# Performance work log

Hardware: AMD Instinct MI355X
Metric: run time of the kernel (lower is better)

The kernel has to match this reference:

```python
import jax, jax.numpy as jnp
import numpy as np

B, S, D = 16, 2048, 128
NEG = -1e9


def setup_inputs() -> dict:
    key = jax.random.key(0)
    kq, kk, kv = jax.random.split(key, 3)
    queries = jax.random.normal(kq, (B, S, D), dtype=jnp.float32)
    keys = jax.random.normal(kk, (B, S, D), dtype=jnp.float32)
    values = jax.random.normal(kv, (B, S, D), dtype=jnp.float32)
    # causal additive mask: 0 on/below diagonal, -1e9 above
    causal = jnp.triu(jnp.ones((S, S), dtype=jnp.float32), k=1) * NEG
    return {"queries": queries, "keys": keys, "values": values, "mask": causal}


def reference(queries, keys, values, mask):
    d = queries.shape[-1]
    scale = 1.0 / jnp.sqrt(jnp.asarray(d, dtype=queries.dtype))
    # scores: [b, q, k]
    scores = jnp.einsum("bqd,bkd->bqk", queries, keys) * scale
    scores = scores + mask  # broadcast [S,S] over batch
    weights = jax.nn.softmax(scores, axis=-1)
    # dropout p=0.0 in eval mode -> identity
    return jnp.einsum("bqk,bkd->bqd", weights, values)
```

## Files before the change

### kernel.cpp

```cpp
#include <hip/hip_runtime.h>
#include <hip/hip_bf16.h>

#define SS   2048
#define DD   128
#define QBLK 64
#define KBLK 64

typedef __attribute__((ext_vector_type(8))) short short8;
typedef __attribute__((ext_vector_type(4))) float f32x4;

__device__ __forceinline__ unsigned short f2bf(float x) {
  return __builtin_bit_cast(unsigned short, (__bf16)x);
}

__device__ __forceinline__ int sigma_col(int a) {
  return (a & 35) | ((a & 12) << 1) | ((a & 16) >> 2);
}

__global__ __launch_bounds__(256) void sdpa_causal_kernel(
    const float* __restrict__ Q, const float* __restrict__ K,
    const float* __restrict__ V, float* __restrict__ O)
{
  __shared__ __align__(16) char smem[KBLK * DD * 2 + DD * KBLK * 2];
  char* Klds  = smem;
  char* Vtlds = smem + KBLK * DD * 2;

  const int b   = blockIdx.x;
  const int qb  = (int)gridDim.y - 1 - (int)blockIdx.y;
  const int q0  = qb * QBLK;
  const int tid = threadIdx.x;
  const int lane = tid & 63;
  const int wid  = tid >> 6;
  const int l15  = lane & 15;
  const int hi   = lane >> 4;

  const float* Qb = Q + (size_t)b * SS * DD;
  const float* Kb = K + (size_t)b * SS * DD;
  const float* Vb = V + (size_t)b * SS * DD;
  float*       Ob = O + (size_t)b * SS * DD;

  const float scale = 0.08838834764831845f;

  short8 qf[4];
  {
    const float* qrow = Qb + (size_t)(q0 + wid * 16 + l15) * DD;
    #pragma unroll
    for (int c = 0; c < 4; ++c) {
      const float4* p = reinterpret_cast<const float4*>(qrow + 32 * c + 8 * hi);
      float4 x = p[0], y = p[1];
      short8 w;
      w[0] = f2bf(x.x * scale); w[1] = f2bf(x.y * scale);
      w[2] = f2bf(x.z * scale); w[3] = f2bf(x.w * scale);
      w[4] = f2bf(y.x * scale); w[5] = f2bf(y.y * scale);
      w[6] = f2bf(y.z * scale); w[7] = f2bf(y.w * scale);
      qf[c] = w;
    }
  }

  f32x4 o[8];
  #pragma unroll
  for (int nt = 0; nt < 8; ++nt) o[nt] = (f32x4){0.f, 0.f, 0.f, 0.f};
  float m = -INFINITY;
  float lsum = 0.f;

  const int ntile = qb + 1;
  for (int t = 0; t < ntile; ++t) {
    const int kv0 = t * KBLK;
    if (t) __syncthreads();

    #pragma unroll
    for (int u = 0; u < 4; ++u) {
      int row = u * 16 + (tid >> 4);
      int col = 8 * (tid & 15);
      const float4* sp = reinterpret_cast<const float4*>(Kb + (size_t)(kv0 + row) * DD + col);
      float4 x = sp[0], y = sp[1];
      short8 w;
      w[0] = f2bf(x.x); w[1] = f2bf(x.y); w[2] = f2bf(x.z); w[3] = f2bf(x.w);
      w[4] = f2bf(y.x); w[5] = f2bf(y.y); w[6] = f2bf(y.z); w[7] = f2bf(y.w);
      int byteoff = row * 256 + col * 2;
      byteoff ^= (row & 7) << 4;
      *reinterpret_cast<short8*>(Klds + byteoff) = w;
    }
    #pragma unroll
    for (int u = 0; u < 4; ++u) {
      int row = u * 16 + (tid >> 4);
      int col = 8 * (tid & 15);
      const float4* sp = reinterpret_cast<const float4*>(Vb + (size_t)(kv0 + row) * DD + col);
      float4 x = sp[0], y = sp[1];
      int sc = sigma_col(row);
      float vals[8] = {x.x, x.y, x.z, x.w, y.x, y.y, y.z, y.w};
      #pragma unroll
      for (int j = 0; j < 8; ++j) {
        int d = col + j;
        int byteoff = (d << 7) + (sc << 1);
        byteoff ^= (((d >> 3) ^ d) & 7) << 4;
        *reinterpret_cast<unsigned short*>(Vtlds + byteoff) = f2bf(vals[j]);
      }
    }
    __syncthreads();

    f32x4 sacc[4];
    #pragma unroll
    for (int g = 0; g < 4; ++g) {
      f32x4 acc = {0.f, 0.f, 0.f, 0.f};
      #pragma unroll
      for (int c = 0; c < 4; ++c) {
        int row = g * 16 + l15;
        int byteoff = row * 256 + (32 * c + 8 * hi) * 2;
        byteoff ^= (row & 7) << 4;
        short8 kf = *reinterpret_cast<const short8*>(Klds + byteoff);
        acc = __builtin_amdgcn_mfma_f32_16x16x32_bf16(kf, qf[c], acc, 0, 0, 0);
      }
      sacc[g] = acc;
    }

    if (t == ntile - 1) {
      const int q = q0 + wid * 16 + l15;
      #pragma unroll
      for (int g = 0; g < 4; ++g)
        #pragma unroll
        for (int i = 0; i < 4; ++i) {
          int key = kv0 + g * 16 + 4 * hi + i;
          if (key > q) sacc[g][i] = -1e30f;
        }
    }

    float tmax = -INFINITY;
    #pragma unroll
    for (int g = 0; g < 4; ++g)
      #pragma unroll
      for (int i = 0; i < 4; ++i) tmax = fmaxf(tmax, sacc[g][i]);
    tmax = fmaxf(tmax, __shfl_xor(tmax, 16));
    tmax = fmaxf(tmax, __shfl_xor(tmax, 32));
    float mnew = fmaxf(m, tmax);
    float corr = __expf(m - mnew);
    m = mnew;

    float p[4][4];
    float psum = 0.f;
    #pragma unroll
    for (int g = 0; g < 4; ++g)
      #pragma unroll
      for (int i = 0; i < 4; ++i) {
        float pv = __expf(sacc[g][i] - mnew);
        p[g][i] = pv;
        psum += pv;
      }
    psum += __shfl_xor(psum, 16);
    psum += __shfl_xor(psum, 32);
    lsum = lsum * corr + psum;

    float corrO[4];
    #pragma unroll
    for (int i = 0; i < 4; ++i) corrO[i] = __shfl(corr, 4 * hi + i);
    #pragma unroll
    for (int nt = 0; nt < 8; ++nt)
      #pragma unroll
      for (int i = 0; i < 4; ++i) o[nt][i] *= corrO[i];

    short8 pf[2];
    #pragma unroll
    for (int ks = 0; ks < 2; ++ks) {
      short8 w;
      #pragma unroll
      for (int i = 0; i < 4; ++i) {
        w[i]     = f2bf(p[2 * ks][i]);
        w[4 + i] = f2bf(p[2 * ks + 1][i]);
      }
      pf[ks] = w;
    }

    #pragma unroll
    for (int ks = 0; ks < 2; ++ks) {
      #pragma unroll
      for (int nt = 0; nt < 8; ++nt) {
        int d = nt * 16 + l15;
        int byteoff = (d << 7) + (ks * 32 + 8 * hi) * 2;
        byteoff ^= (((d >> 3) ^ d) & 7) << 4;
        short8 vf = *reinterpret_cast<const short8*>(Vtlds + byteoff);
        o[nt] = __builtin_amdgcn_mfma_f32_16x16x32_bf16(pf[ks], vf, o[nt], 0, 0, 0);
      }
    }
  }

  float rl = 1.0f / lsum;
  float rlO[4];
  #pragma unroll
  for (int i = 0; i < 4; ++i) rlO[i] = __shfl(rl, 4 * hi + i);
  const int qrow = q0 + wid * 16;
  #pragma unroll
  for (int nt = 0; nt < 8; ++nt)
    #pragma unroll
    for (int i = 0; i < 4; ++i)
      Ob[(size_t)(qrow + 4 * hi + i) * DD + nt * 16 + l15] = o[nt][i] * rlO[i];
}

extern "C" void kernel_launch(void* const* d_in, const int* in_sizes, int n_in,
                              void* d_out, int out_size, void* d_ws, size_t ws_size,
                              hipStream_t stream) {
  const float* Q = (const float*)d_in[0];
  const float* K = (const float*)d_in[1];
  const float* V = (const float*)d_in[2];
  float* O = (float*)d_out;

  dim3 grid(16, SS / QBLK);
  dim3 block(256);
  sdpa_causal_kernel<<<grid, block, 0, stream>>>(Q, K, V, O);
}
```

Measured before the change: 71.96 us.

## Prepack K/V to bf16 swizzled tiles and double-buffer async LDS loads

A prepass kernel converts K and V to bf16 once per call and writes them into workspace in the LDS-swizzled layout, with V already transposed. The attention kernel then copies tiles straight into LDS with global_load_lds, double-buffered so the next tile loads while the current one computes. It also reorders the q-block schedule and raises wave priority around the MFMA sections. This removes the conversion and transpose work that was repeated per query block, at the cost of an extra launch and workspace traffic, and it only runs when the workspace is large enough.

```diff
diff --git a/kernel.cpp b/kernel.cpp
--- a/kernel.cpp
+++ b/kernel.cpp
@@ -1,10 +1,14 @@
 #include <hip/hip_runtime.h>
 #include <hip/hip_bf16.h>
+#include <cstdint>
 
 #define SS   2048
 #define DD   128
 #define QBLK 64
 #define KBLK 64
+#define NTILES (SS / KBLK)
+#define TILE_BYTES 16384
+#define WS_NEED ((size_t)16 * NTILES * TILE_BYTES * 2)
 
 typedef __attribute__((ext_vector_type(8))) short short8;
 typedef __attribute__((ext_vector_type(4))) float f32x4;
@@ -15,6 +19,237 @@
 
 __device__ __forceinline__ int sigma_col(int a) {
   return (a & 35) | ((a & 12) << 1) | ((a & 16) >> 2);
+}
+
+__global__ __launch_bounds__(256) void prepack_kv(
+    const float* __restrict__ K, const float* __restrict__ V, char* __restrict__ ws)
+{
+  __shared__ float vf[64][129];
+  const int b = blockIdx.x, t = blockIdx.y;
+  const int tid = threadIdx.x;
+  const float* Kt = K + ((size_t)b * SS + t * KBLK) * DD;
+  const float* Vt = V + ((size_t)b * SS + t * KBLK) * DD;
+  char* Kd = ws + ((size_t)(b * NTILES + t)) * TILE_BYTES;
+  char* Vd = ws + (size_t)16 * NTILES * TILE_BYTES + ((size_t)(b * NTILES + t)) * TILE_BYTES;
+
+  #pragma unroll
+  for (int u = 0; u < 4; ++u) {
+    int row = u * 16 + (tid >> 4);
+    int col = 8 * (tid & 15);
+    const float4* sp = reinterpret_cast<const float4*>(Kt + (size_t)row * DD + col);
+    float4 x = sp[0], y = sp[1];
+    short8 w;
+    w[0] = f2bf(x.x); w[1] = f2bf(x.y); w[2] = f2bf(x.z); w[3] = f2bf(x.w);
+    w[4] = f2bf(y.x); w[5] = f2bf(y.y); w[6] = f2bf(y.z); w[7] = f2bf(y.w);
+    int off = (row * 256 + col * 2) ^ ((row & 7) << 4);
+    *reinterpret_cast<short8*>(Kd + off) = w;
+  }
+  #pragma unroll
+  for (int u = 0; u < 4; ++u) {
+    int row = u * 16 + (tid >> 4);
+    int col = 8 * (tid & 15);
+    const float4* sp = reinterpret_cast<const float4*>(Vt + (size_t)row * DD + col);
+    float4 x = sp[0], y = sp[1];
+    vf[row][col + 0] = x.x; vf[row][col + 1] = x.y; vf[row][col + 2] = x.z; vf[row][col + 3] = x.w;
+    vf[row][col + 4] = y.x; vf[row][col + 5] = y.y; vf[row][col + 6] = y.z; vf[row][col + 7] = y.w;
+  }
+  __syncthreads();
+  #pragma unroll
+  for (int q = 0; q < 4; ++q) {
+    int idx = q * 256 + tid;
+    int d = idx >> 3, y = idx & 7;
+    short8 w;
+    #pragma unroll
+    for (int j = 0; j < 8; ++j) {
+      int a = (j & 3) | ((y & 3) << 2) | ((j & 4) << 2) | ((y & 4) << 3);
+      w[j] = f2bf(vf[a][d]);
+    }
+    int off = ((d << 7) + (y << 4)) ^ ((((d >> 3) ^ d) & 7) << 4);
+    *reinterpret_cast<short8*>(Vd + off) = w;
+  }
+}
+
+__device__ __forceinline__ void stage_tile(const char* Ksrc, const char* Vsrc,
+                                           char* Kl, char* Vl, int wid, int lane)
+{
+  #pragma unroll
+  for (int i = 0; i < 4; ++i) {
+    int off = wid * 4096 + i * 1024;
+    __builtin_amdgcn_global_load_lds(
+        (const __attribute__((address_space(1))) unsigned int*)(Ksrc + off + lane * 16),
+        (__attribute__((address_space(3))) unsigned int*)(Kl + off), 16, 0, 0);
+  }
+  #pragma unroll
+  for (int i = 0; i < 4; ++i) {
+    int off = wid * 4096 + i * 1024;
+    __builtin_amdgcn_global_load_lds(
+        (const __attribute__((address_space(1))) unsigned int*)(Vsrc + off + lane * 16),
+        (__attribute__((address_space(3))) unsigned int*)(Vl + off), 16, 0, 0);
+  }
+}
+
+__global__ __launch_bounds__(256) void sdpa_causal_v2(
+    const float* __restrict__ Q, const char* __restrict__ ws, float* __restrict__ O)
+{
+  __shared__ __align__(16) char smem[2 * 32768];
+
+  const int b = blockIdx.x;
+  const int y = blockIdx.y;
+  const int qb = (y < 16) ? (31 - y) : (y - 16);
+  const int q0 = qb * QBLK;
+  const int tid = threadIdx.x;
+  const int lane = tid & 63;
+  const int wid  = tid >> 6;
+  const int l15  = lane & 15;
+  const int hi   = lane >> 4;
+
+  const float* Qb = Q + (size_t)b * SS * DD;
+  float*       Ob = O + (size_t)b * SS * DD;
+  const char*  Kws = ws + ((size_t)b * NTILES) * TILE_BYTES;
+  const char*  Vws = ws + (size_t)16 * NTILES * TILE_BYTES + ((size_t)b * NTILES) * TILE_BYTES;
+
+  const float scale = 0.08838834764831845f;
+
+  short8 qf[4];
+  {
+    const float* qrow = Qb + (size_t)(q0 + wid * 16 + l15) * DD;
+    #pragma unroll
+    for (int c = 0; c < 4; ++c) {
+      const float4* p = reinterpret_cast<const float4*>(qrow + 32 * c + 8 * hi);
+      float4 x = p[0], y2 = p[1];
+      short8 w;
+      w[0] = f2bf(x.x * scale); w[1] = f2bf(x.y * scale);
+      w[2] = f2bf(x.z * scale); w[3] = f2bf(x.w * scale);
+      w[4] = f2bf(y2.x * scale); w[5] = f2bf(y2.y * scale);
+      w[6] = f2bf(y2.z * scale); w[7] = f2bf(y2.w * scale);
+      qf[c] = w;
+    }
+  }
+
+  f32x4 o[8];
+  #pragma unroll
+  for (int nt = 0; nt < 8; ++nt) o[nt] = (f32x4){0.f, 0.f, 0.f, 0.f};
+  float m = -INFINITY;
+  float lsum = 0.f;
+
+  const int ntile = qb + 1;
+  int cur = 0;
+
+  stage_tile(Kws, Vws, smem, smem + 16384, wid, lane);
+  __syncthreads();
+
+  for (int t = 0; t < ntile; ++t) {
+    if (t + 1 < ntile) {
+      char* nb = smem + (cur ^ 1) * 32768;
+      stage_tile(Kws + (size_t)(t + 1) * TILE_BYTES, Vws + (size_t)(t + 1) * TILE_BYTES,
+                 nb, nb + 16384, wid, lane);
+    }
+
+    const char* Kl = smem + cur * 32768;
+    const char* Vl = Kl + 16384;
+    const int kv0 = t * KBLK;
+
+    f32x4 sacc[4];
+    __builtin_amdgcn_s_setprio(1);
+    #pragma unroll
+    for (int g = 0; g < 4; ++g) {
+      f32x4 acc = {0.f, 0.f, 0.f, 0.f};
+      #pragma unroll
+      for (int c = 0; c < 4; ++c) {
+        int row = g * 16 + l15;
+        int byteoff = (row * 256 + (32 * c + 8 * hi) * 2) ^ ((row & 7) << 4);
+        short8 kf = *reinterpret_cast<const short8*>(Kl + byteoff);
+        acc = __builtin_amdgcn_mfma_f32_16x16x32_bf16(kf, qf[c], acc, 0, 0, 0);
+      }
+      sacc[g] = acc;
+    }
+    __builtin_amdgcn_s_setprio(0);
+
+    if (t == ntile - 1) {
+      const int q = q0 + wid * 16 + l15;
+      #pragma unroll
+      for (int g = 0; g < 4; ++g)
+        #pragma unroll
+        for (int i = 0; i < 4; ++i) {
+          int key = kv0 + g * 16 + 4 * hi + i;
+          if (key > q) sacc[g][i] = -1e30f;
+        }
+    }
+
+    float tmax = -INFINITY;
+    #pragma unroll
+    for (int g = 0; g < 4; ++g)
+      #pragma unroll
+      for (int i = 0; i < 4; ++i) tmax = fmaxf(tmax, sacc[g][i]);
+    tmax = fmaxf(tmax, __shfl_xor(tmax, 16));
+    tmax = fmaxf(tmax, __shfl_xor(tmax, 32));
+    float mnew = fmaxf(m, tmax);
+    float corr = __expf(m - mnew);
+    m = mnew;
+
+    float p[4][4];
+    float psum = 0.f;
+    #pragma unroll
+    for (int g = 0; g < 4; ++g)
+      #pragma unroll
+      for (int i = 0; i < 4; ++i) {
+        float pv = __expf(sacc[g][i] - mnew);
+        p[g][i] = pv;
+        psum += pv;
+      }
+    psum += __shfl_xor(psum, 16);
+    psum += __shfl_xor(psum, 32);
+    lsum = lsum * corr + psum;
+
+    float corrO[4];
+    #pragma unroll
+    for (int i = 0; i < 4; ++i) corrO[i] = __shfl(corr, 4 * hi + i);
+    #pragma unroll
+    for (int nt = 0; nt < 8; ++nt)
+      #pragma unroll
+      for (int i = 0; i < 4; ++i) o[nt][i] *= corrO[i];
+
+    short8 pf[2];
+    #pragma unroll
+    for (int ks = 0; ks < 2; ++ks) {
+      short8 w;
+      #pragma unroll
+      for (int i = 0; i < 4; ++i) {
+        w[i]     = f2bf(p[2 * ks][i]);
+        w[4 + i] = f2bf(p[2 * ks + 1][i]);
+      }
+      pf[ks] = w;
+    }
+
+    __builtin_amdgcn_s_setprio(1);
+    #pragma unroll
+    for (int ks = 0; ks < 2; ++ks) {
+      #pragma unroll
+      for (int nt = 0; nt < 8; ++nt) {
+        int d = nt * 16 + l15;
+        int byteoff = ((d << 7) + (ks * 32 + 8 * hi) * 2) ^ ((((d >> 3) ^ d) & 7) << 4);
+        short8 vvf = *reinterpret_cast<const short8*>(Vl + byteoff);
+        o[nt] = __builtin_amdgcn_mfma_f32_16x16x32_bf16(pf[ks], vvf, o[nt], 0, 0, 0);
+      }
+    }
+    __builtin_amdgcn_s_setprio(0);
+
+    if (t + 1 < ntile) {
+      __syncthreads();
+      cur ^= 1;
+    }
+  }
+
+  float rl = 1.0f / lsum;
+  float rlO[4];
+  #pragma unroll
+  for (int i = 0; i < 4; ++i) rlO[i] = __shfl(rl, 4 * hi + i);
+  const int qrow = q0 + wid * 16;
+  #pragma unroll
+  for (int nt = 0; nt < 8; ++nt)
+    #pragma unroll
+    for (int i = 0; i < 4; ++i)
+      Ob[(size_t)(qrow + 4 * hi + i) * DD + nt * 16 + l15] = o[nt][i] * rlO[i];
 }
 
 __global__ __launch_bounds__(256) void sdpa_causal_kernel(
@@ -77,8 +312,7 @@
       short8 w;
       w[0] = f2bf(x.x); w[1] = f2bf(x.y); w[2] = f2bf(x.z); w[3] = f2bf(x.w);
       w[4] = f2bf(y.x); w[5] = f2bf(y.y); w[6] = f2bf(y.z); w[7] = f2bf(y.w);
-      int byteoff = row * 256 + col * 2;
-      byteoff ^= (row & 7) << 4;
+      int byteoff = (row * 256 + col * 2) ^ ((row & 7) << 4);
       *reinterpret_cast<short8*>(Klds + byteoff) = w;
     }
     #pragma unroll
@@ -92,8 +326,7 @@
       #pragma unroll
       for (int j = 0; j < 8; ++j) {
         int d = col + j;
-        int byteoff = (d << 7) + (sc << 1);
-        byteoff ^= (((d >> 3) ^ d) & 7) << 4;
+        int byteoff = ((d << 7) + (sc << 1)) ^ ((((d >> 3) ^ d) & 7) << 4);
         *reinterpret_cast<unsigned short*>(Vtlds + byteoff) = f2bf(vals[j]);
       }
     }
@@ -106,8 +339,7 @@
       #pragma unroll
       for (int c = 0; c < 4; ++c) {
         int row = g * 16 + l15;
-        int byteoff = row * 256 + (32 * c + 8 * hi) * 2;
-        byteoff ^= (row & 7) << 4;
+        int byteoff = (row * 256 + (32 * c + 8 * hi) * 2) ^ ((row & 7) << 4);
         short8 kf = *reinterpret_cast<const short8*>(Klds + byteoff);
         acc = __builtin_amdgcn_mfma_f32_16x16x32_bf16(kf, qf[c], acc, 0, 0, 0);
       }
@@ -175,10 +407,9 @@
       #pragma unroll
       for (int nt = 0; nt < 8; ++nt) {
         int d = nt * 16 + l15;
-        int byteoff = (d << 7) + (ks * 32 + 8 * hi) * 2;
-        byteoff ^= (((d >> 3) ^ d) & 7) << 4;
-        short8 vf = *reinterpret_cast<const short8*>(Vtlds + byteoff);
-        o[nt] = __builtin_amdgcn_mfma_f32_16x16x32_bf16(pf[ks], vf, o[nt], 0, 0, 0);
+        int byteoff = ((d << 7) + (ks * 32 + 8 * hi) * 2) ^ ((((d >> 3) ^ d) & 7) << 4);
+        short8 vvf = *reinterpret_cast<const short8*>(Vtlds + byteoff);
+        o[nt] = __builtin_amdgcn_mfma_f32_16x16x32_bf16(pf[ks], vvf, o[nt], 0, 0, 0);
       }
     }
   }
@@ -203,7 +434,11 @@
   const float* V = (const float*)d_in[2];
   float* O = (float*)d_out;
 
-  dim3 grid(16, SS / QBLK);
-  dim3 block(256);
-  sdpa_causal_kernel<<<grid, block, 0, stream>>>(Q, K, V, O);
-}
+  if (ws_size >= WS_NEED) {
+    char* ws = (char*)d_ws;
+    prepack_kv<<<dim3(16, NTILES), 256, 0, stream>>>(K, V, ws);
+    sdpa_causal_v2<<<dim3(16, 32), 256, 0, stream>>>(Q, ws, O);
+  } else {
+    sdpa_causal_kernel<<<dim3(16, 32), 256, 0, stream>>>(Q, K, V, O);
+  }
+}
```

Result: faster. 64.81 us (-9.9%).
